# Kernel optimization log

Hardware: AMD Instinct MI355X
Metric: run time of the kernel (lower is better)

The kernel has to match this reference:

```python
import jax, jax.numpy as jnp
import numpy as np

T, B, I, H, L = 512, 64, 512, 1024, 2


def setup_inputs() -> dict:
    key = jax.random.key(0)
    ks = jax.random.split(key, 11)
    s = 0.03  # keep tanh recurrence in a sane range
    return {
        "x": jax.random.normal(ks[0], (T, B, I), jnp.float32),
        "hidden": jnp.zeros((L, B, H), jnp.float32),
        "W_ih0": jax.random.normal(ks[1], (H, I), jnp.float32) * s,
        "W_hh0": jax.random.normal(ks[2], (H, H), jnp.float32) * s,
        "b_ih0": jax.random.normal(ks[3], (H,), jnp.float32) * s,
        "b_hh0": jax.random.normal(ks[4], (H,), jnp.float32) * s,
        "W_ih1": jax.random.normal(ks[5], (H, H), jnp.float32) * s,
        "W_hh1": jax.random.normal(ks[6], (H, H), jnp.float32) * s,
        "b_ih1": jax.random.normal(ks[7], (H,), jnp.float32) * s,
        "b_hh1": jax.random.normal(ks[8], (H,), jnp.float32) * s,
        "W_fc": jax.random.normal(ks[9], (I, H), jnp.float32) * s,
        "b_fc": jax.random.normal(ks[10], (I,), jnp.float32) * s,
    }


def _rnn_layer(x_proj, h0, W_hh, b_hh):
    # x_proj: [T, B, H] = x @ W_ih.T + b_ih, precomputed as one big GEMM.
    # h_t = tanh(x_proj_t + h_{t-1} @ W_hh.T + b_hh)
    def step(h, xp):
        h_new = jnp.tanh(xp + h @ W_hh.T + b_hh)
        return h_new, h_new
    _, ys = jax.lax.scan(step, h0, x_proj)
    return ys  # [T, B, H]


def reference(x, hidden, W_ih0, W_hh0, b_ih0, b_hh0,
              W_ih1, W_hh1, b_ih1, b_hh1, W_fc, b_fc):
    # Layer 0 (input -> hidden), then layer 1 (hidden -> hidden), tanh RNN.
    out0 = _rnn_layer(jnp.einsum("tbi,hi->tbh", x, W_ih0) + b_ih0,
                      hidden[0], W_hh0, b_hh0)
    out1 = _rnn_layer(jnp.einsum("tbh,gh->tbg", out0, W_ih1) + b_ih1,
                      hidden[1], W_hh1, b_hh1)
    # Trailing Linear(hidden_dim_rnn -> input_size) applied per timestep.
    return jnp.einsum("tbh,ih->tbi", out1, W_fc) + b_fc
```

## Files before the change

kernel.cpp:

```cpp
#include <hip/hip_runtime.h>
#include <stdint.h>

#define T_DIM 512
#define B_DIM 64
#define I_DIM 512
#define H_DIM 1024
#define BH ((size_t)B_DIM * H_DIM)
#define NW0 32
#define NW1 32

typedef __attribute__((ext_vector_type(8))) short short8;
typedef __attribute__((ext_vector_type(4))) float f32x4;

__device__ __forceinline__ unsigned short f2bf(float f) {
    unsigned int u = __float_as_uint(f);
    unsigned int r = (u + 0x7FFFu + ((u >> 16) & 1u)) >> 16;
    return (unsigned short)r;
}
__device__ __forceinline__ float bf2f(unsigned short b) {
    return __uint_as_float(((unsigned int)b) << 16);
}
__device__ __forceinline__ float fast_tanh(float x) {
    x = fminf(fmaxf(x, -15.f), 15.f);
    float e = __expf(2.f * x);
    return (e - 1.f) / (e + 1.f);
}

__device__ __forceinline__ unsigned long long ld64_sys(const unsigned short* p) {
    return __hip_atomic_load((const unsigned long long*)p, __ATOMIC_RELAXED,
                             __HIP_MEMORY_SCOPE_AGENT);
}
__device__ __forceinline__ short8 ldA_sys(const unsigned short* p) {
    union { unsigned long long u[2]; short8 v; } t;
    t.u[0] = ld64_sys(p);
    t.u[1] = ld64_sys(p + 4);
    return t.v;
}
__device__ __forceinline__ void st64_sys(unsigned short* p, unsigned long long v) {
    __hip_atomic_store((unsigned long long*)p, v, __ATOMIC_RELAXED,
                       __HIP_MEMORY_SCOPE_AGENT);
}
__device__ __forceinline__ void spin1(const int* f) {
    while (__hip_atomic_load(f, __ATOMIC_RELAXED, __HIP_MEMORY_SCOPE_AGENT) == 0)
        __builtin_amdgcn_s_sleep(1);
}

__global__ void conv_f2bf(const float* __restrict__ in, unsigned short* __restrict__ out, int n4) {
    int i = blockIdx.x * blockDim.x + threadIdx.x;
    int stride = gridDim.x * blockDim.x;
    for (int idx = i; idx < n4; idx += stride) {
        float4 v = reinterpret_cast<const float4*>(in)[idx];
        ushort4 o;
        o.x = f2bf(v.x); o.y = f2bf(v.y); o.z = f2bf(v.z); o.w = f2bf(v.w);
        reinterpret_cast<ushort4*>(out)[idx] = o;
    }
}

__global__ void bias_sum(const float* __restrict__ a, const float* __restrict__ b,
                         float* __restrict__ o, int n) {
    int i = blockIdx.x * blockDim.x + threadIdx.x;
    if (i < n) o[i] = a[i] + b[i];
}

template <int OUT_BF16>
__global__ void gemm_bias(const unsigned short* __restrict__ A,
                          const unsigned short* __restrict__ W,
                          const float* __restrict__ bias,
                          void* __restrict__ Cout,
                          int M, int N, int K) {
    const int ntn = N >> 6;
    const int mt = blockIdx.x / ntn;
    const int nt = blockIdx.x % ntn;
    const int m_base = mt << 6, n_base = nt << 6;
    const int lane = threadIdx.x & 63;
    const int wave = threadIdx.x >> 6;
    const int wm = wave >> 1, wn = wave & 1;
    const int r0 = lane & 15;
    const int g  = lane >> 4;
    const int koff = g << 3;

    f32x4 acc[2][2];
    for (int i = 0; i < 2; i++)
        for (int j = 0; j < 2; j++)
            acc[i][j] = (f32x4)(0.f);

    const unsigned short* Arow0 = A + (size_t)(m_base + wm * 32 + r0) * K + koff;
    const unsigned short* Wrow0 = W + (size_t)(n_base + wn * 32 + r0) * K + koff;

    for (int k0 = 0; k0 < K; k0 += 32) {
        short8 a0 = *reinterpret_cast<const short8*>(Arow0 + k0);
        short8 a1 = *reinterpret_cast<const short8*>(Arow0 + (size_t)16 * K + k0);
        short8 b0 = *reinterpret_cast<const short8*>(Wrow0 + k0);
        short8 b1 = *reinterpret_cast<const short8*>(Wrow0 + (size_t)16 * K + k0);
        acc[0][0] = __builtin_amdgcn_mfma_f32_16x16x32_bf16(a0, b0, acc[0][0], 0, 0, 0);
        acc[0][1] = __builtin_amdgcn_mfma_f32_16x16x32_bf16(a0, b1, acc[0][1], 0, 0, 0);
        acc[1][0] = __builtin_amdgcn_mfma_f32_16x16x32_bf16(a1, b0, acc[1][0], 0, 0, 0);
        acc[1][1] = __builtin_amdgcn_mfma_f32_16x16x32_bf16(a1, b1, acc[1][1], 0, 0, 0);
    }

    for (int mi = 0; mi < 2; mi++) {
        for (int ni = 0; ni < 2; ni++) {
            for (int r = 0; r < 4; r++) {
                int row = m_base + wm * 32 + mi * 16 + g * 4 + r;
                int col = n_base + wn * 32 + ni * 16 + r0;
                float v = acc[mi][ni][r] + bias[col];
                if (OUT_BF16)
                    ((unsigned short*)Cout)[(size_t)row * N + col] = f2bf(v);
                else
                    ((float*)Cout)[(size_t)row * N + col] = v;
            }
        }
    }
}

__global__ void __launch_bounds__(256, 1)
rnn_persist(const unsigned short* __restrict__ xp0,
            const unsigned short* __restrict__ whh0,
            const unsigned short* __restrict__ wih1,
            const unsigned short* __restrict__ whh1,
            const float* __restrict__ bias1,
            const unsigned short* __restrict__ hinit,
            unsigned short* __restrict__ out0,
            unsigned short* __restrict__ out1,
            int* __restrict__ flags0,
            int* __restrict__ flags1)
{
    __shared__ __attribute__((aligned(16))) char smem[140288];
    const int tid  = threadIdx.x;
    const int lane = tid & 63;
    const int wave = tid >> 6;
    const int r0 = lane & 15;
    const int g  = lane >> 4;
    const int wg = blockIdx.x;
    const int brow = (wave << 4) + r0;

    const char* Bp = smem + (g << 9) + (r0 << 4);
    float* sc = (float*)(smem + 131072) + wave * 576;
    const int rr = lane >> 2;
    const int cc = (lane & 3) << 3;
    const int orow = (wave << 4) + rr;

    if (wg < NW0) {
        const int n0 = wg << 5;
        for (int i = tid; i < 4096; i += 256) {
            const int c = i & 31, kc = i >> 5;
            *reinterpret_cast<short8*>(smem + (((kc << 5) + c) << 4)) =
                *reinterpret_cast<const short8*>(whh0 + (size_t)(n0 + c) * H_DIM + (kc << 3));
        }
        __syncthreads();
        const int gcol = n0 + cc;

        for (int t = 0; t < T_DIM; ++t) {
            if (t) {
                if (tid < 32) spin1(&flags0[(size_t)(t - 1) * 32 + tid]);
                __syncthreads();
            }
            const unsigned short* hp = t ? out0 + (size_t)(t - 1) * BH : hinit;
            const unsigned short* Ap = hp + (size_t)brow * H_DIM + (g << 3);
            f32x4 acc[2][4];
            #pragma unroll
            for (int a = 0; a < 2; ++a)
                #pragma unroll
                for (int b = 0; b < 4; ++b) acc[a][b] = (f32x4)(0.f);
            short8 ar[16];
            #pragma unroll
            for (int h = 0; h < 2; ++h) {
                #pragma unroll
                for (int i = 0; i < 16; ++i)
                    ar[i] = ldA_sys(Ap + ((h * 16 + i) << 5));
                #pragma unroll
                for (int i = 0; i < 16; ++i) {
                    const char* bp = Bp + (size_t)(h * 16 + i) * 2048;
                    short8 b0 = *reinterpret_cast<const short8*>(bp);
                    short8 b1 = *reinterpret_cast<const short8*>(bp + 256);
                    acc[0][i & 3] = __builtin_amdgcn_mfma_f32_16x16x32_bf16(ar[i], b0, acc[0][i & 3], 0, 0, 0);
                    acc[1][i & 3] = __builtin_amdgcn_mfma_f32_16x16x32_bf16(ar[i], b1, acc[1][i & 3], 0, 0, 0);
                }
            }
            f32x4 s0 = (acc[0][0] + acc[0][1]) + (acc[0][2] + acc[0][3]);
            f32x4 s1 = (acc[1][0] + acc[1][1]) + (acc[1][2] + acc[1][3]);
            #pragma unroll
            for (int r = 0; r < 4; ++r) {
                sc[(g * 4 + r) * 36 + r0]      = s0[r];
                sc[(g * 4 + r) * 36 + 16 + r0] = s1[r];
            }
            __builtin_amdgcn_sched_barrier(0);
            f32x4 t0 = *reinterpret_cast<const f32x4*>(sc + rr * 36 + cc);
            f32x4 t1 = *reinterpret_cast<const f32x4*>(sc + rr * 36 + cc + 4);
            short8 xv = *reinterpret_cast<const short8*>(
                xp0 + (size_t)t * BH + (size_t)orow * H_DIM + gcol);
            float v[8];
            #pragma unroll
            for (int j = 0; j < 4; ++j) {
                v[j]     = fast_tanh(t0[j] + bf2f((unsigned short)xv[j]));
                v[4 + j] = fast_tanh(t1[j] + bf2f((unsigned short)xv[4 + j]));
            }
            unsigned long long lo = (unsigned long long)f2bf(v[0])
                | ((unsigned long long)f2bf(v[1]) << 16)
                | ((unsigned long long)f2bf(v[2]) << 32)
                | ((unsigned long long)f2bf(v[3]) << 48);
            unsigned long long hi = (unsigned long long)f2bf(v[4])
                | ((unsigned long long)f2bf(v[5]) << 16)
                | ((unsigned long long)f2bf(v[6]) << 32)
                | ((unsigned long long)f2bf(v[7]) << 48);
            unsigned short* o = out0 + (size_t)t * BH + (size_t)orow * H_DIM + gcol;
            st64_sys(o, lo);
            st64_sys(o + 4, hi);
            __syncthreads();
            if (tid == 0)
                __hip_atomic_store(&flags0[(size_t)t * 32 + wg], 1,
                                   __ATOMIC_RELAXED, __HIP_MEMORY_SCOPE_AGENT);
        }
    } else {
        const int wg2 = wg - NW0;
        const int n0 = wg2 << 5;
        for (int i = tid; i < 8192; i += 256) {
            const int c = i & 31, kc = i >> 5;
            const unsigned short* src = (kc < 128)
                ? wih1 + (size_t)(n0 + c) * H_DIM + (kc << 3)
                : whh1 + (size_t)(n0 + c) * H_DIM + ((kc - 128) << 3);
            *reinterpret_cast<short8*>(smem + (((kc << 5) + c) << 4)) =
                *reinterpret_cast<const short8*>(src);
        }
        __syncthreads();
        const int gcol = n0 + cc;
        const float4 bv0 = *reinterpret_cast<const float4*>(bias1 + gcol);
        const float4 bv1 = *reinterpret_cast<const float4*>(bias1 + gcol + 4);

        for (int t = 0; t < T_DIM; ++t) {
            if (tid < 32) spin1(&flags0[(size_t)t * 32 + tid]);
            else if (t && tid < 64) spin1(&flags1[(size_t)(t - 1) * 32 + (tid - 32)]);
            __syncthreads();
            const unsigned short* a0 = out0 + (size_t)t * BH;
            const unsigned short* h1 = t ? out1 + (size_t)(t - 1) * BH : hinit + BH;
            const unsigned short* ApA = a0 + (size_t)brow * H_DIM + (g << 3);
            const unsigned short* ApH = h1 + (size_t)brow * H_DIM + (g << 3);
            f32x4 acc[2][4];
            #pragma unroll
            for (int a = 0; a < 2; ++a)
                #pragma unroll
                for (int b = 0; b < 4; ++b) acc[a][b] = (f32x4)(0.f);
            short8 ar[16];
            #pragma unroll
            for (int h = 0; h < 4; ++h) {
                const unsigned short* Ap = (h < 2) ? ApA : ApH;
                const int base = (h & 1) << 4;
                #pragma unroll
                for (int i = 0; i < 16; ++i)
                    ar[i] = ldA_sys(Ap + ((base + i) << 5));
                #pragma unroll
                for (int i = 0; i < 16; ++i) {
                    const char* bp = Bp + (size_t)(h * 16 + i) * 2048;
                    short8 b0 = *reinterpret_cast<const short8*>(bp);
                    short8 b1 = *reinterpret_cast<const short8*>(bp + 256);
                    acc[0][i & 3] = __builtin_amdgcn_mfma_f32_16x16x32_bf16(ar[i], b0, acc[0][i & 3], 0, 0, 0);
                    acc[1][i & 3] = __builtin_amdgcn_mfma_f32_16x16x32_bf16(ar[i], b1, acc[1][i & 3], 0, 0, 0);
                }
            }
            f32x4 s0 = (acc[0][0] + acc[0][1]) + (acc[0][2] + acc[0][3]);
            f32x4 s1 = (acc[1][0] + acc[1][1]) + (acc[1][2] + acc[1][3]);
            #pragma unroll
            for (int r = 0; r < 4; ++r) {
                sc[(g * 4 + r) * 36 + r0]      = s0[r];
                sc[(g * 4 + r) * 36 + 16 + r0] = s1[r];
            }
            __builtin_amdgcn_sched_barrier(0);
            f32x4 t0 = *reinterpret_cast<const f32x4*>(sc + rr * 36 + cc);
            f32x4 t1 = *reinterpret_cast<const f32x4*>(sc + rr * 36 + cc + 4);
            float v[8];
            v[0] = fast_tanh(t0[0] + bv0.x); v[1] = fast_tanh(t0[1] + bv0.y);
            v[2] = fast_tanh(t0[2] + bv0.z); v[3] = fast_tanh(t0[3] + bv0.w);
            v[4] = fast_tanh(t1[0] + bv1.x); v[5] = fast_tanh(t1[1] + bv1.y);
            v[6] = fast_tanh(t1[2] + bv1.z); v[7] = fast_tanh(t1[3] + bv1.w);
            unsigned long long lo = (unsigned long long)f2bf(v[0])
                | ((unsigned long long)f2bf(v[1]) << 16)
                | ((unsigned long long)f2bf(v[2]) << 32)
                | ((unsigned long long)f2bf(v[3]) << 48);
            unsigned long long hi = (unsigned long long)f2bf(v[4])
                | ((unsigned long long)f2bf(v[5]) << 16)
                | ((unsigned long long)f2bf(v[6]) << 32)
                | ((unsigned long long)f2bf(v[7]) << 48);
            unsigned short* o = out1 + (size_t)t * BH + (size_t)orow * H_DIM + gcol;
            st64_sys(o, lo);
            st64_sys(o + 4, hi);
            __syncthreads();
            if (tid == 0)
                __hip_atomic_store(&flags1[(size_t)t * 32 + wg2], 1,
                                   __ATOMIC_RELAXED, __HIP_MEMORY_SCOPE_AGENT);
        }
    }
}

extern "C" void kernel_launch(void* const* d_in, const int* in_sizes, int n_in,
                              void* d_out, int out_size, void* d_ws, size_t ws_size,
                              hipStream_t stream) {
    const float* x      = (const float*)d_in[0];
    const float* hidden = (const float*)d_in[1];
    const float* W_ih0  = (const float*)d_in[2];
    const float* W_hh0  = (const float*)d_in[3];
    const float* b_ih0  = (const float*)d_in[4];
    const float* b_hh0  = (const float*)d_in[5];
    const float* W_ih1  = (const float*)d_in[6];
    const float* W_hh1  = (const float*)d_in[7];
    const float* b_ih1  = (const float*)d_in[8];
    const float* b_hh1  = (const float*)d_in[9];
    const float* W_fc   = (const float*)d_in[10];
    const float* b_fc   = (const float*)d_in[11];

    char* ws = (char*)d_ws;
    size_t off = 0;
    auto alloc = [&](size_t bytes) -> char* {
        char* p = ws + off;
        off += (bytes + 255) & ~(size_t)255;
        return p;
    };
    const size_t TBH = (size_t)T_DIM * B_DIM * H_DIM;
    const size_t TBI = (size_t)T_DIM * B_DIM * I_DIM;

    unsigned short* xb     = (unsigned short*)alloc(TBI * 2);
    unsigned short* wih0b  = (unsigned short*)alloc((size_t)H_DIM * I_DIM * 2);
    unsigned short* whh0b  = (unsigned short*)alloc((size_t)H_DIM * H_DIM * 2);
    unsigned short* wih1b  = (unsigned short*)alloc((size_t)H_DIM * H_DIM * 2);
    unsigned short* whh1b  = (unsigned short*)alloc((size_t)H_DIM * H_DIM * 2);
    unsigned short* wfcb   = (unsigned short*)alloc((size_t)I_DIM * H_DIM * 2);
    unsigned short* hinitb = (unsigned short*)alloc((size_t)2 * B_DIM * H_DIM * 2);
    float* bias0 = (float*)alloc(H_DIM * 4);
    float* bias1 = (float*)alloc(H_DIM * 4);
    unsigned short* xp0    = (unsigned short*)alloc(TBH * 2);
    unsigned short* out0b  = (unsigned short*)alloc(TBH * 2);
    unsigned short* out1b  = (unsigned short*)alloc(TBH * 2);
    int* flags0 = (int*)alloc((size_t)T_DIM * 32 * 4);
    int* flags1 = (int*)alloc((size_t)T_DIM * 32 * 4);

    auto conv = [&](const float* in, unsigned short* out, int n) {
        int n4 = n / 4;
        int blocks = (n4 + 255) / 256;
        if (blocks > 2048) blocks = 2048;
        conv_f2bf<<<blocks, 256, 0, stream>>>(in, out, n4);
    };
    conv(x, xb, (int)TBI);
    conv(W_ih0, wih0b, H_DIM * I_DIM);
    conv(W_hh0, whh0b, H_DIM * H_DIM);
    conv(W_ih1, wih1b, H_DIM * H_DIM);
    conv(W_fc, wfcb, I_DIM * H_DIM);
    conv(hidden, hinitb, 2 * B_DIM * H_DIM);
    conv(W_hh1, whh1b, H_DIM * H_DIM);
    bias_sum<<<4, 256, 0, stream>>>(b_ih0, b_hh0, bias0, H_DIM);
    bias_sum<<<4, 256, 0, stream>>>(b_ih1, b_hh1, bias1, H_DIM);

    (void)hipMemsetAsync(flags0, 0, (size_t)T_DIM * 32 * 4 * 2, stream);

    {
        int M = T_DIM * B_DIM, N = H_DIM, K = I_DIM;
        dim3 grid((M / 64) * (N / 64));
        gemm_bias<1><<<grid, 256, 0, stream>>>(xb, wih0b, bias0, xp0, M, N, K);
    }

    {
        void* args[] = {(void*)&xp0, (void*)&whh0b, (void*)&wih1b, (void*)&whh1b,
                        (void*)&bias1, (void*)&hinitb, (void*)&out0b, (void*)&out1b,
                        (void*)&flags0, (void*)&flags1};
        (void)hipLaunchCooperativeKernel(reinterpret_cast<void*>(rnn_persist),
                                         dim3(NW0 + NW1), dim3(256), args, 0, stream);
    }

    {
        int M = T_DIM * B_DIM, N = I_DIM, K = H_DIM;
        dim3 grid((M / 64) * (N / 64));
        gemm_bias<0><<<grid, 256, 0, stream>>>(out1b, wfcb, b_fc, d_out, M, N, K);
    }
}
```

Before: 8.748 ms.

## Replace per-element atomic loads/stores with plain loads, write-through stores and acquire fence

Hidden-state reads inside the persistent recurrent kernel switch from pairs of 64-bit agent-scope atomic loads to plain 128-bit vector loads. Visibility is restored by an agent-scope acquire fence after each flag barrier. Outputs are written with a single 128-bit write-through store (sc0 sc1) followed by an explicit vmcnt drain before the flag is set. The spin sleep interval is also lengthened. This aims to cut per-step memory instruction count and latency on the serial critical path, at the cost of relying on fence and cache-bypass semantics for correctness.

```diff
diff --git a/kernel.cpp b/kernel.cpp
--- a/kernel.cpp
+++ b/kernel.cpp
@@ -26,23 +26,22 @@
     return (e - 1.f) / (e + 1.f);
 }
 
-__device__ __forceinline__ unsigned long long ld64_sys(const unsigned short* p) {
-    return __hip_atomic_load((const unsigned long long*)p, __ATOMIC_RELAXED,
-                             __HIP_MEMORY_SCOPE_AGENT);
-}
-__device__ __forceinline__ short8 ldA_sys(const unsigned short* p) {
-    union { unsigned long long u[2]; short8 v; } t;
-    t.u[0] = ld64_sys(p);
-    t.u[1] = ld64_sys(p + 4);
-    return t.v;
-}
-__device__ __forceinline__ void st64_sys(unsigned short* p, unsigned long long v) {
-    __hip_atomic_store((unsigned long long*)p, v, __ATOMIC_RELAXED,
-                       __HIP_MEMORY_SCOPE_AGENT);
+__device__ __forceinline__ void st128_wt(unsigned short* p, short8 v) {
+    asm volatile("global_store_dwordx4 %0, %1, off sc0 sc1" :: "v"(p), "v"(v) : "memory");
+}
+__device__ __forceinline__ void acquire_inv() {
+#if __has_builtin(__builtin_amdgcn_fence)
+    __builtin_amdgcn_fence(__ATOMIC_ACQUIRE, "agent");
+#else
+    __threadfence();
+#endif
+}
+__device__ __forceinline__ void drain_stores() {
+    asm volatile("s_waitcnt vmcnt(0)" ::: "memory");
 }
 __device__ __forceinline__ void spin1(const int* f) {
     while (__hip_atomic_load(f, __ATOMIC_RELAXED, __HIP_MEMORY_SCOPE_AGENT) == 0)
-        __builtin_amdgcn_s_sleep(1);
+        __builtin_amdgcn_s_sleep(4);
 }
 
 __global__ void conv_f2bf(const float* __restrict__ in, unsigned short* __restrict__ out, int n4) {
@@ -154,6 +153,7 @@
             if (t) {
                 if (tid < 32) spin1(&flags0[(size_t)(t - 1) * 32 + tid]);
                 __syncthreads();
+                acquire_inv();
             }
             const unsigned short* hp = t ? out0 + (size_t)(t - 1) * BH : hinit;
             const unsigned short* Ap = hp + (size_t)brow * H_DIM + (g << 3);
@@ -167,7 +167,7 @@
             for (int h = 0; h < 2; ++h) {
                 #pragma unroll
                 for (int i = 0; i < 16; ++i)
-                    ar[i] = ldA_sys(Ap + ((h * 16 + i) << 5));
+                    ar[i] = *reinterpret_cast<const short8*>(Ap + ((h * 16 + i) << 5));
                 #pragma unroll
                 for (int i = 0; i < 16; ++i) {
                     const char* bp = Bp + (size_t)(h * 16 + i) * 2048;
@@ -189,23 +189,14 @@
             f32x4 t1 = *reinterpret_cast<const f32x4*>(sc + rr * 36 + cc + 4);
             short8 xv = *reinterpret_cast<const short8*>(
                 xp0 + (size_t)t * BH + (size_t)orow * H_DIM + gcol);
-            float v[8];
+            short8 ov;
             #pragma unroll
             for (int j = 0; j < 4; ++j) {
-                v[j]     = fast_tanh(t0[j] + bf2f((unsigned short)xv[j]));
-                v[4 + j] = fast_tanh(t1[j] + bf2f((unsigned short)xv[4 + j]));
-            }
-            unsigned long long lo = (unsigned long long)f2bf(v[0])
-                | ((unsigned long long)f2bf(v[1]) << 16)
-                | ((unsigned long long)f2bf(v[2]) << 32)
-                | ((unsigned long long)f2bf(v[3]) << 48);
-            unsigned long long hi = (unsigned long long)f2bf(v[4])
-                | ((unsigned long long)f2bf(v[5]) << 16)
-                | ((unsigned long long)f2bf(v[6]) << 32)
-                | ((unsigned long long)f2bf(v[7]) << 48);
-            unsigned short* o = out0 + (size_t)t * BH + (size_t)orow * H_DIM + gcol;
-            st64_sys(o, lo);
-            st64_sys(o + 4, hi);
+                ov[j]     = (short)f2bf(fast_tanh(t0[j] + bf2f((unsigned short)xv[j])));
+                ov[4 + j] = (short)f2bf(fast_tanh(t1[j] + bf2f((unsigned short)xv[4 + j])));
+            }
+            st128_wt(out0 + (size_t)t * BH + (size_t)orow * H_DIM + gcol, ov);
+            drain_stores();
             __syncthreads();
             if (tid == 0)
                 __hip_atomic_store(&flags0[(size_t)t * 32 + wg], 1,
@@ -231,6 +222,7 @@
             if (tid < 32) spin1(&flags0[(size_t)t * 32 + tid]);
             else if (t && tid < 64) spin1(&flags1[(size_t)(t - 1) * 32 + (tid - 32)]);
             __syncthreads();
+            acquire_inv();
             const unsigned short* a0 = out0 + (size_t)t * BH;
             const unsigned short* h1 = t ? out1 + (size_t)(t - 1) * BH : hinit + BH;
             const unsigned short* ApA = a0 + (size_t)brow * H_DIM + (g << 3);
@@ -247,7 +239,7 @@
                 const int base = (h & 1) << 4;
                 #pragma unroll
                 for (int i = 0; i < 16; ++i)
-                    ar[i] = ldA_sys(Ap + ((base + i) << 5));
+                    ar[i] = *reinterpret_cast<const short8*>(Ap + ((base + i) << 5));
                 #pragma unroll
                 for (int i = 0; i < 16; ++i) {
                     const char* bp = Bp + (size_t)(h * 16 + i) * 2048;
@@ -267,22 +259,17 @@
             __builtin_amdgcn_sched_barrier(0);
             f32x4 t0 = *reinterpret_cast<const f32x4*>(sc + rr * 36 + cc);
             f32x4 t1 = *reinterpret_cast<const f32x4*>(sc + rr * 36 + cc + 4);
-            float v[8];
-            v[0] = fast_tanh(t0[0] + bv0.x); v[1] = fast_tanh(t0[1] + bv0.y);
-            v[2] = fast_tanh(t0[2] + bv0.z); v[3] = fast_tanh(t0[3] + bv0.w);
-            v[4] = fast_tanh(t1[0] + bv1.x); v[5] = fast_tanh(t1[1] + bv1.y);
-            v[6] = fast_tanh(t1[2] + bv1.z); v[7] = fast_tanh(t1[3] + bv1.w);
-            unsigned long long lo = (unsigned long long)f2bf(v[0])
-                | ((unsigned long long)f2bf(v[1]) << 16)
-                | ((unsigned long long)f2bf(v[2]) << 32)
-                | ((unsigned long long)f2bf(v[3]) << 48);
-            unsigned long long hi = (unsigned long long)f2bf(v[4])
-                | ((unsigned long long)f2bf(v[5]) << 16)
-                | ((unsigned long long)f2bf(v[6]) << 32)
-                | ((unsigned long long)f2bf(v[7]) << 48);
-            unsigned short* o = out1 + (size_t)t * BH + (size_t)orow * H_DIM + gcol;
-            st64_sys(o, lo);
-            st64_sys(o + 4, hi);
+            short8 ov;
+            ov[0] = (short)f2bf(fast_tanh(t0[0] + bv0.x));
+            ov[1] = (short)f2bf(fast_tanh(t0[1] + bv0.y));
+            ov[2] = (short)f2bf(fast_tanh(t0[2] + bv0.z));
+            ov[3] = (short)f2bf(fast_tanh(t0[3] + bv0.w));
+            ov[4] = (short)f2bf(fast_tanh(t1[0] + bv1.x));
+            ov[5] = (short)f2bf(fast_tanh(t1[1] + bv1.y));
+            ov[6] = (short)f2bf(fast_tanh(t1[2] + bv1.z));
+            ov[7] = (short)f2bf(fast_tanh(t1[3] + bv1.w));
+            st128_wt(out1 + (size_t)t * BH + (size_t)orow * H_DIM + gcol, ov);
+            drain_stores();
             __syncthreads();
             if (tid == 0)
                 __hip_atomic_store(&flags1[(size_t)t * 32 + wg2], 1,
```

New measurement: 7.325 ms. -16.3%, faster.
